# Optimization experiments

Hardware: AMD Instinct MI355X
Metric: run time of the kernel (lower is better)

## Reference

```python
import jax, jax.numpy as jnp
import numpy as np

N = 8192      # num nodes
IN = 256      # in_channels
HID = 128     # hidden_channels
DEG = 32      # avg degree
E = N * DEG   # num edges (without self loops)
EPS_NORM = 1e-12
EPS_SOFTMAX = 1e-16


def setup_inputs() -> dict:
    key = jax.random.key(0)
    ks = jax.random.split(key, 8)
    x = jax.random.normal(ks[0], (N, IN), jnp.float32)
    # random sparse graph with no self loops (PyG AGNNConv removes then re-adds them)
    dst = jax.random.randint(ks[1], (E,), 0, N)
    off = jax.random.randint(ks[2], (E,), 1, N)
    src = (dst + off) % N
    edge_index = jnp.stack([src, dst]).astype(jnp.int32)  # [2, E]
    adj = jnp.zeros((N, N), jnp.float32).at[src, dst].set(1.0)  # dense H used in final mm
    s1 = 1.0 / np.sqrt(IN)
    s2 = 1.0 / np.sqrt(HID)
    W1 = jax.random.uniform(ks[3], (HID, IN), jnp.float32, -s1, s1)
    b1 = jax.random.uniform(ks[4], (HID,), jnp.float32, -s1, s1)
    W2 = jax.random.uniform(ks[5], (HID, HID), jnp.float32, -s2, s2)
    b2 = jax.random.uniform(ks[6], (HID,), jnp.float32, -s2, s2)
    beta2 = jnp.ones((1,), jnp.float32)  # learnable beta of prop2 (init 1.0)
    return dict(x=x, adj=adj, edge_index=edge_index, W1=W1, b1=b1, W2=W2, b2=b2, beta2=beta2)


def _agnn(x, src, dst, beta):
    # L2 normalize (F.normalize, eps=1e-12)
    norm = jnp.sqrt(jnp.sum(x * x, axis=-1, keepdims=True))
    xn = x / jnp.maximum(norm, EPS_NORM)
    # cosine-similarity attention score per edge, scaled by beta
    alpha = beta * jnp.sum(xn[src] * xn[dst], axis=-1)        # [E']
    # softmax over edges grouped by destination node (PyG softmax)
    m = jax.ops.segment_max(alpha, dst, num_segments=N)       # [N]
    e = jnp.exp(alpha - m[dst])
    s = jax.ops.segment_sum(e, dst, num_segments=N)           # [N]
    w = e / (s[dst] + EPS_SOFTMAX)                            # [E']
    # scatter-add weighted source features
    return jax.ops.segment_sum(x[src] * w[:, None], dst, num_segments=N)


def reference(x, adj, edge_index, W1, b1, W2, b2, beta2):
    # eval mode: dropout(p=0.5) is identity
    h = jax.nn.relu(x @ W1.T + b1)                            # [N, HID]
    # add self loops (edge_index is guaranteed self-loop free)
    loops = jnp.arange(N, dtype=edge_index.dtype)
    src = jnp.concatenate([edge_index[0], loops])
    dst = jnp.concatenate([edge_index[1], loops])
    h = _agnn(h, src, dst, jnp.float32(1.0))                  # prop1: fixed beta=1
    h = _agnn(h, src, dst, beta2[0])                          # prop2: learnable beta
    h = jax.nn.relu(h @ W2.T + b2)                            # [N, HID]
    return adj @ h                                            # torch.mm(H, x)
```

## Files before the change

### kernel.cpp

```cpp
#include <hip/hip_runtime.h>
#include <stdint.h>

typedef unsigned long long u64;

#define IN_C 256
#define HID_C 128
#define SRC_CAP 192
#define MM_CAP 256

__device__ __align__(256) unsigned char g_fallback[40u << 20];

__global__ void k_zero128(uint4* __restrict__ p, int n16) {
  int i = blockIdx.x * blockDim.x + threadIdx.x;
  int stride = gridDim.x * blockDim.x;
  uint4 z = make_uint4(0u, 0u, 0u, 0u);
  for (; i < n16; i += stride) p[i] = z;
}

__device__ inline void gemm_body(int bid, int tid,
                                 const float* __restrict__ X, const float* __restrict__ W,
                                 const float* __restrict__ b, float* __restrict__ C, int K,
                                 float* __restrict__ ssq_out, float* __restrict__ invn_out,
                                 float (*Ws)[HID_C + 4], float (*Xs)[64]) {
  const int rl = tid >> 5;
  const int cg = tid & 31;
  const int row0 = bid * 16;
  float4 acc0 = make_float4(0.f, 0.f, 0.f, 0.f);
  float4 acc1 = make_float4(0.f, 0.f, 0.f, 0.f);
  for (int kt = 0; kt < K; kt += 64) {
    for (int idx = tid; idx < HID_C * 16; idx += 256) {
      int c = idx >> 4, kq = idx & 15;
      const float4 w4 = *(const float4*)&W[c * K + kt + kq * 4];
      Ws[kq * 4 + 0][c] = w4.x;
      Ws[kq * 4 + 1][c] = w4.y;
      Ws[kq * 4 + 2][c] = w4.z;
      Ws[kq * 4 + 3][c] = w4.w;
    }
    {
      int r = tid >> 4, kq = tid & 15;
      const float4 x4 = *(const float4*)&X[(row0 + r) * K + kt + kq * 4];
      *(float4*)&Xs[r][kq * 4] = x4;
    }
    __syncthreads();
#pragma unroll 16
    for (int kk = 0; kk < 64; ++kk) {
      const float4 w = *(const float4*)&Ws[kk][cg * 4];
      const float x0 = Xs[rl * 2 + 0][kk];
      const float x1 = Xs[rl * 2 + 1][kk];
      acc0.x = fmaf(w.x, x0, acc0.x); acc0.y = fmaf(w.y, x0, acc0.y);
      acc0.z = fmaf(w.z, x0, acc0.z); acc0.w = fmaf(w.w, x0, acc0.w);
      acc1.x = fmaf(w.x, x1, acc1.x); acc1.y = fmaf(w.y, x1, acc1.y);
      acc1.z = fmaf(w.z, x1, acc1.z); acc1.w = fmaf(w.w, x1, acc1.w);
    }
    __syncthreads();
  }
  const float4 bb = *(const float4*)&b[cg * 4];
  float4 o0, o1;
  o0.x = fmaxf(acc0.x + bb.x, 0.f); o0.y = fmaxf(acc0.y + bb.y, 0.f);
  o0.z = fmaxf(acc0.z + bb.z, 0.f); o0.w = fmaxf(acc0.w + bb.w, 0.f);
  o1.x = fmaxf(acc1.x + bb.x, 0.f); o1.y = fmaxf(acc1.y + bb.y, 0.f);
  o1.z = fmaxf(acc1.z + bb.z, 0.f); o1.w = fmaxf(acc1.w + bb.w, 0.f);
  int r0 = row0 + rl * 2;
  *(float4*)&C[r0 * HID_C + cg * 4] = o0;
  *(float4*)&C[(r0 + 1) * HID_C + cg * 4] = o1;
  if (ssq_out) {
    float s0 = o0.x * o0.x + o0.y * o0.y + o0.z * o0.z + o0.w * o0.w;
    float s1 = o1.x * o1.x + o1.y * o1.y + o1.z * o1.z + o1.w * o1.w;
#pragma unroll
    for (int off = 16; off >= 1; off >>= 1) {
      s0 += __shfl_xor(s0, off, 64);
      s1 += __shfl_xor(s1, off, 64);
    }
    if (cg == 0) {
      ssq_out[r0] = s0;
      ssq_out[r0 + 1] = s1;
      invn_out[r0] = 1.0f / fmaxf(sqrtf(s0), 1e-12f);
      invn_out[r0 + 1] = 1.0f / fmaxf(sqrtf(s1), 1e-12f);
    }
  }
}

__global__ __launch_bounds__(256) void k_build_gemm(
    const float* __restrict__ X, const float* __restrict__ W, const float* __restrict__ b,
    float* __restrict__ C, int K, float* __restrict__ ssq_out, float* __restrict__ invn_out,
    int nblk_gemm,
    const int* __restrict__ src, const int* __restrict__ dst, int E,
    u64* __restrict__ bmT, u64* __restrict__ bmS, int wpr,
    u64* __restrict__ duplist, int* __restrict__ dupcnt, int dupcap) {
  __shared__ float Ws[64][HID_C + 4];
  __shared__ float Xs[16][64];
  if ((int)blockIdx.x < nblk_gemm) {
    gemm_body(blockIdx.x, threadIdx.x, X, W, b, C, K, ssq_out, invn_out, Ws, Xs);
    return;
  }
  int e = (blockIdx.x - nblk_gemm) * 256 + threadIdx.x;
  if (e < E) {
    int s = src[e], d = dst[e];
    u64 bit = 1ull << (s & 63);
    u64 old = atomicOr(&bmT[(size_t)d * wpr + (s >> 6)], bit);
    if (old & bit) {
      int i = atomicAdd(dupcnt, 1);
      if (i < dupcap) duplist[i] = ((u64)(uint32_t)d << 32) | (uint32_t)s;
    }
    atomicOr(&bmS[(size_t)s * wpr + (d >> 6)], 1ull << (d & 63));
  }
}

__global__ __launch_bounds__(256) void k_gemm_relu(
    const float* __restrict__ X, const float* __restrict__ W,
    const float* __restrict__ b, float* __restrict__ C, int K,
    float* __restrict__ ssq_out, float* __restrict__ invn_out) {
  __shared__ float Ws[64][HID_C + 4];
  __shared__ float Xs[16][64];
  gemm_body(blockIdx.x, threadIdx.x, X, W, b, C, K, ssq_out, invn_out, Ws, Xs);
}

__global__ void k_agg(const float* __restrict__ hin, float* __restrict__ hout,
                      const u64* __restrict__ bmT, int wpr,
                      const u64* __restrict__ duplist, const int* __restrict__ dupcnt, int dupcap,
                      int* __restrict__ glist, int* __restrict__ gdeg, int enumerate,
                      const float* __restrict__ invn, const float* __restrict__ ssq,
                      const float* __restrict__ beta_ptr,
                      float* __restrict__ ssq_out, float* __restrict__ invn_out,
                      int n) {
  __shared__ int s_src[4][SRC_CAP];
  int wv = threadIdx.x >> 6;
  int wid = (blockIdx.x * blockDim.x + threadIdx.x) >> 6;
  int lane = threadIdx.x & 63;
  if (wid >= n) return;
  int* S = s_src[wv];
  int M;

  if (enumerate) {
    const u64* row = bmT + (size_t)wid * wpr;
    u64 w0 = row[lane];
    u64 w1 = row[64 + lane];
    int c = __popcll(w0) + __popcll(w1);
    int incl = c;
#pragma unroll
    for (int off = 1; off < 64; off <<= 1) {
      int v = __shfl_up(incl, off, 64);
      if (lane >= off) incl += v;
    }
    M = __shfl(incl, 63, 64);
    int pos = incl - c;
    u64 t = w0;
    while (t) {
      int bp = __ffsll(t) - 1; t &= t - 1;
      if (pos < SRC_CAP) S[pos] = (lane << 6) + bp;
      pos++;
    }
    t = w1;
    while (t) {
      int bp = __ffsll(t) - 1; t &= t - 1;
      if (pos < SRC_CAP) S[pos] = ((64 + lane) << 6) + bp;
      pos++;
    }
    if (M > SRC_CAP) M = SRC_CAP;
    int D = min(*dupcnt, dupcap);
    for (int base = 0; base < D; base += 64) {
      int m = min(64, D - base);
      bool match = false; int sE = 0x7fffffff;
      if (lane < m) {
        u64 ent = duplist[base + lane];
        if ((int)(ent >> 32) == wid) { match = true; sE = (int)(uint32_t)ent; }
      }
      while (__ballot(match)) {
        int sv = match ? sE : 0x7fffffff;
#pragma unroll
        for (int o = 32; o >= 1; o >>= 1) sv = min(sv, __shfl_xor(sv, o, 64));
        int cnt = (int)__popcll(__ballot(match && sE == sv));
        if (lane < cnt && M + lane < SRC_CAP) S[M + lane] = sv;
        M = min(M + cnt, SRC_CAP);
        if (match && sE == sv) match = false;
      }
    }
    for (int i = lane; i < M; i += 64) glist[wid * SRC_CAP + i] = S[i];
    if (lane == 0) gdeg[wid] = M;
  } else {
    M = gdeg[wid];
    for (int i = lane; i < M; i += 64) S[i] = glist[wid * SRC_CAP + i];
  }

  float beta = beta_ptr ? beta_ptr[0] : 1.0f;
  float invd = invn[wid];
  float eloop = __expf(beta * (ssq[wid] * invd) * invd);

  const int g = lane >> 4;
  const int gl = lane & 15;
  const float* qrow = &hin[wid * HID_C + gl * 8];
  float4 qa = *(const float4*)&qrow[0];
  float4 qb = *(const float4*)&qrow[4];
  float4 A0, A1;
  float esum;
  if (g == 0) {
    A0 = make_float4(eloop * qa.x, eloop * qa.y, eloop * qa.z, eloop * qa.w);
    A1 = make_float4(eloop * qb.x, eloop * qb.y, eloop * qb.z, eloop * qb.w);
    esum = eloop;
  } else {
    A0 = make_float4(0.f, 0.f, 0.f, 0.f);
    A1 = make_float4(0.f, 0.f, 0.f, 0.f);
    esum = 0.f;
  }
  for (int e0 = 0; e0 < M; e0 += 4) {
    int e = e0 + g;
    bool valid = (e < M);
    int s = S[valid ? e : e0];
    const float* r = &hin[s * HID_C + gl * 8];
    float4 ra = *(const float4*)&r[0];
    float4 rb = *(const float4*)&r[4];
    float d = qa.x * ra.x + qa.y * ra.y + qa.z * ra.z + qa.w * ra.w +
              qb.x * rb.x + qb.y * rb.y + qb.z * rb.z + qb.w * rb.w;
#pragma unroll
    for (int off = 1; off <= 8; off <<= 1) d += __shfl_xor(d, off, 64);
    float w = valid ? __expf(beta * d * invd * invn[s]) : 0.f;
    esum += w;
    A0.x = fmaf(w, ra.x, A0.x); A0.y = fmaf(w, ra.y, A0.y);
    A0.z = fmaf(w, ra.z, A0.z); A0.w = fmaf(w, ra.w, A0.w);
    A1.x = fmaf(w, rb.x, A1.x); A1.y = fmaf(w, rb.y, A1.y);
    A1.z = fmaf(w, rb.z, A1.z); A1.w = fmaf(w, rb.w, A1.w);
  }
#pragma unroll
  for (int off = 16; off <= 32; off <<= 1) {
    esum += __shfl_xor(esum, off, 64);
    A0.x += __shfl_xor(A0.x, off, 64); A0.y += __shfl_xor(A0.y, off, 64);
    A0.z += __shfl_xor(A0.z, off, 64); A0.w += __shfl_xor(A0.w, off, 64);
    A1.x += __shfl_xor(A1.x, off, 64); A1.y += __shfl_xor(A1.y, off, 64);
    A1.z += __shfl_xor(A1.z, off, 64); A1.w += __shfl_xor(A1.w, off, 64);
  }
  float winv = 1.0f / (esum + 1e-16f);
  A0.x *= winv; A0.y *= winv; A0.z *= winv; A0.w *= winv;
  A1.x *= winv; A1.y *= winv; A1.z *= winv; A1.w *= winv;
  if (g == 0) {
    float* orow = &hout[wid * HID_C + gl * 8];
    *(float4*)&orow[0] = A0;
    *(float4*)&orow[4] = A1;
    if (ssq_out) {
      float s = A0.x * A0.x + A0.y * A0.y + A0.z * A0.z + A0.w * A0.w +
                A1.x * A1.x + A1.y * A1.y + A1.z * A1.z + A1.w * A1.w;
#pragma unroll
      for (int off = 1; off <= 8; off <<= 1) s += __shfl_xor(s, off, 64);
      if (gl == 0) {
        ssq_out[wid] = s;
        invn_out[wid] = 1.0f / fmaxf(sqrtf(s), 1e-12f);
      }
    }
  }
}

__global__ void k_mm_bits(const u64* __restrict__ bm, const float* __restrict__ h,
                          float* __restrict__ out, int n, int wpr) {
  __shared__ int s_idx[4][MM_CAP];
  int wv = threadIdx.x >> 6;
  int wid = (blockIdx.x * blockDim.x + threadIdx.x) >> 6;
  int lane = threadIdx.x & 63;
  if (wid >= n) return;
  int* S = s_idx[wv];
  const u64* row = bm + (size_t)wid * wpr;
  u64 w0 = row[lane];
  u64 w1 = row[64 + lane];
  int c = __popcll(w0) + __popcll(w1);
  int incl = c;
#pragma unroll
  for (int off = 1; off < 64; off <<= 1) {
    int v = __shfl_up(incl, off, 64);
    if (lane >= off) incl += v;
  }
  int M = __shfl(incl, 63, 64);
  int pos = incl - c;
  u64 t = w0;
  while (t) {
    int bp = __ffsll(t) - 1; t &= t - 1;
    if (pos < MM_CAP) S[pos] = (lane << 6) + bp;
    pos++;
  }
  t = w1;
  while (t) {
    int bp = __ffsll(t) - 1; t &= t - 1;
    if (pos < MM_CAP) S[pos] = ((64 + lane) << 6) + bp;
    pos++;
  }
  if (M > MM_CAP) M = MM_CAP;
  float2 acc = make_float2(0.f, 0.f);
  int i = 0;
  for (; i + 1 < M; i += 2) {
    int ka = S[i], kb = S[i + 1];
    float2 ha = *(const float2*)&h[ka * HID_C + lane * 2];
    float2 hb = *(const float2*)&h[kb * HID_C + lane * 2];
    acc.x += ha.x + hb.x;
    acc.y += ha.y + hb.y;
  }
  if (i < M) {
    float2 ha = *(const float2*)&h[S[i] * HID_C + lane * 2];
    acc.x += ha.x;
    acc.y += ha.y;
  }
  *(float2*)&out[wid * HID_C + lane * 2] = acc;
}

extern "C" void kernel_launch(void* const* d_in, const int* in_sizes, int n_in,
                              void* d_out, int out_size, void* d_ws, size_t ws_size,
                              hipStream_t stream) {
  const float* x     = (const float*)d_in[0];
  const int*   eio   = (const int*)d_in[2];
  const float* W1    = (const float*)d_in[3];
  const float* b1    = (const float*)d_in[4];
  const float* W2    = (const float*)d_in[5];
  const float* b2    = (const float*)d_in[6];
  const float* beta2 = (const float*)d_in[7];
  float* out = (float*)d_out;

  const int N = in_sizes[0] / IN_C;
  const int E = in_sizes[2] / 2;
  const int WPR = N / 64;
  const int* esrc = eio;
  const int* edst = eio + E;
  const int DUPCAP = E;

  size_t off = 0;
  auto take = [&](size_t bytes) -> size_t {
    size_t o = off;
    off = (off + bytes + 255) & ~(size_t)255;
    return o;
  };
  size_t o_bufA   = take((size_t)N * HID_C * 4);
  size_t o_bufB   = take((size_t)N * HID_C * 4);
  size_t o_invnA  = take((size_t)N * 4);
  size_t o_ssqA   = take((size_t)N * 4);
  size_t o_invnB  = take((size_t)N * 4);
  size_t o_ssqB   = take((size_t)N * 4);
  size_t o_glist  = take((size_t)N * SRC_CAP * 4);
  size_t o_gdeg   = take((size_t)N * 4);
  size_t o_bmT    = take((size_t)N * WPR * 8);
  size_t o_bmS    = take((size_t)N * WPR * 8);
  size_t o_dupcnt = take(256);
  size_t need_zero_end = o_dupcnt + 256;
  size_t o_duplist = take((size_t)DUPCAP * 8);
  size_t need_full = off;

  unsigned char* base = (unsigned char*)d_ws;
  if (ws_size < need_full) {
    void* p = nullptr;
    hipGetSymbolAddress(&p, HIP_SYMBOL(g_fallback));
    base = (unsigned char*)p;
  }

  float* bufA    = (float*)(base + o_bufA);
  float* bufB    = (float*)(base + o_bufB);
  float* invnA   = (float*)(base + o_invnA);
  float* ssqA    = (float*)(base + o_ssqA);
  float* invnB   = (float*)(base + o_invnB);
  float* ssqB    = (float*)(base + o_ssqB);
  int*   glist   = (int*)(base + o_glist);
  int*   gdeg    = (int*)(base + o_gdeg);
  u64*   bmT     = (u64*)(base + o_bmT);
  u64*   bmS     = (u64*)(base + o_bmS);
  int*   dupcnt  = (int*)(base + o_dupcnt);
  u64*   duplist = (u64*)(base + o_duplist);

  dim3 blk(256);

  {
    size_t zbytes = need_zero_end - o_bmT;
    int n16 = (int)(zbytes / 16);
    k_zero128<<<dim3(4096), blk, 0, stream>>>((uint4*)(base + o_bmT), n16);
  }

  {
    int nblk_gemm = N / 16;
    int nblk_build = (E + 255) / 256;
    k_build_gemm<<<dim3(nblk_gemm + nblk_build), blk, 0, stream>>>(
        x, W1, b1, bufA, IN_C, ssqA, invnA, nblk_gemm,
        esrc, edst, E, bmT, bmS, WPR, duplist, dupcnt, DUPCAP);
  }

  k_agg<<<dim3(N / 4), blk, 0, stream>>>(bufA, bufB, bmT, WPR, duplist, dupcnt, DUPCAP,
                                         glist, gdeg, 1,
                                         invnA, ssqA, nullptr, ssqB, invnB, N);

  k_agg<<<dim3(N / 4), blk, 0, stream>>>(bufB, bufA, bmT, WPR, duplist, dupcnt, DUPCAP,
                                         glist, gdeg, 0,
                                         invnB, ssqB, beta2, nullptr, nullptr, N);

  k_gemm_relu<<<dim3(N / 16), blk, 0, stream>>>(bufA, W2, b2, bufB, HID_C, nullptr, nullptr);

  k_mm_bits<<<dim3(N / 4), blk, 0, stream>>>(bmS, bufB, out, N, WPR);
}
```

Baseline: 110.4 us.

## Fuse second AGNN aggregation with W2 linear+ReLU into one kernel

The second propagation kernel now also runs the final linear layer. Each wave writes its normalized aggregated row to shared memory, then the block streams W2 in transposed tiles and computes bias+ReLU outputs directly. This drops the separate GEMM launch and the global round trip of the intermediate features. In exchange every block reloads all of W2 (64 KB) through shared memory for only 4 rows, and the extra block-wide syncs can reduce the overlap between gather and compute.

```diff
diff --git a/kernel.cpp b/kernel.cpp
--- a/kernel.cpp
+++ b/kernel.cpp
@@ -106,21 +106,11 @@
   }
 }
 
-__global__ __launch_bounds__(256) void k_gemm_relu(
-    const float* __restrict__ X, const float* __restrict__ W,
-    const float* __restrict__ b, float* __restrict__ C, int K,
-    float* __restrict__ ssq_out, float* __restrict__ invn_out) {
-  __shared__ float Ws[64][HID_C + 4];
-  __shared__ float Xs[16][64];
-  gemm_body(blockIdx.x, threadIdx.x, X, W, b, C, K, ssq_out, invn_out, Ws, Xs);
-}
-
 __global__ void k_agg(const float* __restrict__ hin, float* __restrict__ hout,
                       const u64* __restrict__ bmT, int wpr,
                       const u64* __restrict__ duplist, const int* __restrict__ dupcnt, int dupcap,
-                      int* __restrict__ glist, int* __restrict__ gdeg, int enumerate,
+                      int* __restrict__ glist, int* __restrict__ gdeg,
                       const float* __restrict__ invn, const float* __restrict__ ssq,
-                      const float* __restrict__ beta_ptr,
                       float* __restrict__ ssq_out, float* __restrict__ invn_out,
                       int n) {
   __shared__ int s_src[4][SRC_CAP];
@@ -131,7 +121,7 @@
   int* S = s_src[wv];
   int M;
 
-  if (enumerate) {
+  {
     const u64* row = bmT + (size_t)wid * wpr;
     u64 w0 = row[lane];
     u64 w1 = row[64 + lane];
@@ -177,14 +167,10 @@
     }
     for (int i = lane; i < M; i += 64) glist[wid * SRC_CAP + i] = S[i];
     if (lane == 0) gdeg[wid] = M;
-  } else {
-    M = gdeg[wid];
-    for (int i = lane; i < M; i += 64) S[i] = glist[wid * SRC_CAP + i];
-  }
-
-  float beta = beta_ptr ? beta_ptr[0] : 1.0f;
+  }
+
   float invd = invn[wid];
-  float eloop = __expf(beta * (ssq[wid] * invd) * invd);
+  float eloop = __expf((ssq[wid] * invd) * invd);
 
   const int g = lane >> 4;
   const int gl = lane & 15;
@@ -213,7 +199,7 @@
               qb.x * rb.x + qb.y * rb.y + qb.z * rb.z + qb.w * rb.w;
 #pragma unroll
     for (int off = 1; off <= 8; off <<= 1) d += __shfl_xor(d, off, 64);
-    float w = valid ? __expf(beta * d * invd * invn[s]) : 0.f;
+    float w = valid ? __expf(d * invd * invn[s]) : 0.f;
     esum += w;
     A0.x = fmaf(w, ra.x, A0.x); A0.y = fmaf(w, ra.y, A0.y);
     A0.z = fmaf(w, ra.z, A0.z); A0.w = fmaf(w, ra.w, A0.w);
@@ -235,17 +221,111 @@
     float* orow = &hout[wid * HID_C + gl * 8];
     *(float4*)&orow[0] = A0;
     *(float4*)&orow[4] = A1;
-    if (ssq_out) {
-      float s = A0.x * A0.x + A0.y * A0.y + A0.z * A0.z + A0.w * A0.w +
-                A1.x * A1.x + A1.y * A1.y + A1.z * A1.z + A1.w * A1.w;
-#pragma unroll
-      for (int off = 1; off <= 8; off <<= 1) s += __shfl_xor(s, off, 64);
-      if (gl == 0) {
-        ssq_out[wid] = s;
-        invn_out[wid] = 1.0f / fmaxf(sqrtf(s), 1e-12f);
-      }
-    }
-  }
+    float s = A0.x * A0.x + A0.y * A0.y + A0.z * A0.z + A0.w * A0.w +
+              A1.x * A1.x + A1.y * A1.y + A1.z * A1.z + A1.w * A1.w;
+#pragma unroll
+    for (int off = 1; off <= 8; off <<= 1) s += __shfl_xor(s, off, 64);
+    if (gl == 0) {
+      ssq_out[wid] = s;
+      invn_out[wid] = 1.0f / fmaxf(sqrtf(s), 1e-12f);
+    }
+  }
+}
+
+__global__ __launch_bounds__(256) void k_agg_mlp(
+    const float* __restrict__ hin, float* __restrict__ hout,
+    const int* __restrict__ glist, const int* __restrict__ gdeg,
+    const float* __restrict__ invn, const float* __restrict__ ssq,
+    const float* __restrict__ beta_ptr,
+    const float* __restrict__ W2, const float* __restrict__ b2, int n) {
+  __shared__ int   s_src[4][SRC_CAP];
+  __shared__ float s_row[4][HID_C];
+  __shared__ float s_w2t[32][HID_C];
+  const int wv = threadIdx.x >> 6;
+  const int wid = (blockIdx.x * blockDim.x + threadIdx.x) >> 6;
+  const int lane = threadIdx.x & 63;
+  int* S = s_src[wv];
+  const int M = gdeg[wid];
+  for (int i = lane; i < M; i += 64) S[i] = glist[wid * SRC_CAP + i];
+
+  const float beta = beta_ptr[0];
+  const float invd = invn[wid];
+  const float eloop = __expf(beta * (ssq[wid] * invd) * invd);
+
+  const int g = lane >> 4;
+  const int gl = lane & 15;
+  const float* qrow = &hin[wid * HID_C + gl * 8];
+  float4 qa = *(const float4*)&qrow[0];
+  float4 qb = *(const float4*)&qrow[4];
+  float4 A0, A1;
+  float esum;
+  if (g == 0) {
+    A0 = make_float4(eloop * qa.x, eloop * qa.y, eloop * qa.z, eloop * qa.w);
+    A1 = make_float4(eloop * qb.x, eloop * qb.y, eloop * qb.z, eloop * qb.w);
+    esum = eloop;
+  } else {
+    A0 = make_float4(0.f, 0.f, 0.f, 0.f);
+    A1 = make_float4(0.f, 0.f, 0.f, 0.f);
+    esum = 0.f;
+  }
+  for (int e0 = 0; e0 < M; e0 += 4) {
+    int e = e0 + g;
+    bool valid = (e < M);
+    int s = S[valid ? e : e0];
+    const float* r = &hin[s * HID_C + gl * 8];
+    float4 ra = *(const float4*)&r[0];
+    float4 rb = *(const float4*)&r[4];
+    float d = qa.x * ra.x + qa.y * ra.y + qa.z * ra.z + qa.w * ra.w +
+              qb.x * rb.x + qb.y * rb.y + qb.z * rb.z + qb.w * rb.w;
+#pragma unroll
+    for (int off = 1; off <= 8; off <<= 1) d += __shfl_xor(d, off, 64);
+    float w = valid ? __expf(beta * d * invd * invn[s]) : 0.f;
+    esum += w;
+    A0.x = fmaf(w, ra.x, A0.x); A0.y = fmaf(w, ra.y, A0.y);
+    A0.z = fmaf(w, ra.z, A0.z); A0.w = fmaf(w, ra.w, A0.w);
+    A1.x = fmaf(w, rb.x, A1.x); A1.y = fmaf(w, rb.y, A1.y);
+    A1.z = fmaf(w, rb.z, A1.z); A1.w = fmaf(w, rb.w, A1.w);
+  }
+#pragma unroll
+  for (int off = 16; off <= 32; off <<= 1) {
+    esum += __shfl_xor(esum, off, 64);
+    A0.x += __shfl_xor(A0.x, off, 64); A0.y += __shfl_xor(A0.y, off, 64);
+    A0.z += __shfl_xor(A0.z, off, 64); A0.w += __shfl_xor(A0.w, off, 64);
+    A1.x += __shfl_xor(A1.x, off, 64); A1.y += __shfl_xor(A1.y, off, 64);
+    A1.z += __shfl_xor(A1.z, off, 64); A1.w += __shfl_xor(A1.w, off, 64);
+  }
+  float winv = 1.0f / (esum + 1e-16f);
+  if (g == 0) {
+    A0.x *= winv; A0.y *= winv; A0.z *= winv; A0.w *= winv;
+    A1.x *= winv; A1.y *= winv; A1.z *= winv; A1.w *= winv;
+    *(float4*)&s_row[wv][gl * 8] = A0;
+    *(float4*)&s_row[wv][gl * 8 + 4] = A1;
+  }
+  __syncthreads();
+
+  float acc0 = b2[lane];
+  float acc1 = b2[lane + 64];
+  const float* row = s_row[wv];
+  for (int kt = 0; kt < HID_C; kt += 32) {
+    for (int i = threadIdx.x; i < HID_C * 8; i += 256) {
+      int c2 = i >> 3, kq = i & 7;
+      const float4 w4 = *(const float4*)&W2[c2 * HID_C + kt + kq * 4];
+      s_w2t[kq * 4 + 0][c2] = w4.x;
+      s_w2t[kq * 4 + 1][c2] = w4.y;
+      s_w2t[kq * 4 + 2][c2] = w4.z;
+      s_w2t[kq * 4 + 3][c2] = w4.w;
+    }
+    __syncthreads();
+#pragma unroll
+    for (int kk = 0; kk < 32; ++kk) {
+      float rv = row[kt + kk];
+      acc0 = fmaf(s_w2t[kk][lane], rv, acc0);
+      acc1 = fmaf(s_w2t[kk][lane + 64], rv, acc1);
+    }
+    __syncthreads();
+  }
+  hout[wid * HID_C + lane] = fmaxf(acc0, 0.f);
+  hout[wid * HID_C + lane + 64] = fmaxf(acc1, 0.f);
 }
 
 __global__ void k_mm_bits(const u64* __restrict__ bm, const float* __restrict__ h,
@@ -375,14 +455,10 @@
   }
 
   k_agg<<<dim3(N / 4), blk, 0, stream>>>(bufA, bufB, bmT, WPR, duplist, dupcnt, DUPCAP,
-                                         glist, gdeg, 1,
-                                         invnA, ssqA, nullptr, ssqB, invnB, N);
-
-  k_agg<<<dim3(N / 4), blk, 0, stream>>>(bufB, bufA, bmT, WPR, duplist, dupcnt, DUPCAP,
-                                         glist, gdeg, 0,
-                                         invnB, ssqB, beta2, nullptr, nullptr, N);
-
-  k_gemm_relu<<<dim3(N / 16), blk, 0, stream>>>(bufA, W2, b2, bufB, HID_C, nullptr, nullptr);
-
-  k_mm_bits<<<dim3(N / 4), blk, 0, stream>>>(bmS, bufB, out, N, WPR);
-}
+                                         glist, gdeg, invnA, ssqA, ssqB, invnB, N);
+
+  k_agg_mlp<<<dim3(N / 4), blk, 0, stream>>>(bufB, bufA, glist, gdeg,
+                                             invnB, ssqB, beta2, W2, b2, N);
+
+  k_mm_bits<<<dim3(N / 4), blk, 0, stream>>>(bmS, bufA, out, N, WPR);
+}
```

After: 179.0 us. 62.1% more time.
